# Kernel tuning notes

Measured on AMD Instinct MI355X. Metric: run time of the kernel, lower is better.

## Reference

```python
import jax, jax.numpy as jnp
import numpy as np

T = 16          # video_length
HEADS = 8
DIM_HEAD = 64
INNER = HEADS * DIM_HEAD   # 512
SCALE = DIM_HEAD ** -0.5
QDIM = 320      # input_dims[0]
NTOK = 1024     # num_tokens[0] == N == M (pose tokens)
CTOK = 256      # context_tokens == per-frame context tokens (16x16)
HC = WC = 16    # sqrt(CTOK)
HM = WM = 32    # after bilinear x2 upsample (sqrt(NTOK))
CDIM = 1024     # context_dim
NBLOCKS = 2
FF_INNER = 4 * QDIM  # 1280, GEGLU proj -> 2*FF_INNER


def _ln(x, w, b):
    mu = jnp.mean(x, axis=-1, keepdims=True)
    var = jnp.mean(jnp.square(x - mu), axis=-1, keepdims=True)
    return (x - mu) * jax.lax.rsqrt(var + 1e-5) * w + b


def setup_inputs() -> dict:
    key = jax.random.key(0)
    ks = jax.random.split(key, 24)
    rn = lambda i, shape, s: jax.random.normal(ks[i], shape, jnp.float32) * s
    return {
        "hidden_state": rn(0, (2 * T, NTOK, HEADS, QDIM // HEADS), 1.0),
        "context": rn(1, (2, 2, CTOK, CDIM), 1.0),
        "pose": rn(2, (2, QDIM, T, HM, WM), 1.0),
        "Wq": rn(3, (NBLOCKS, QDIM, INNER), 0.02),
        "Wk": rn(4, (NBLOCKS, CDIM, INNER), 0.02),
        "Wv": rn(5, (NBLOCKS, CDIM, INNER), 0.02),
        "Wa": rn(6, (NBLOCKS, QDIM, INNER), 0.02),
        "agent_bias": rn(7, (NBLOCKS, NTOK, CTOK), 0.01),
        "query_bias": rn(8, (NBLOCKS, NTOK, NTOK), 0.01),
        "dwc_w": rn(9, (NBLOCKS, INNER, 1, 3, 3), 0.1),
        "dwc_b": rn(10, (NBLOCKS, INNER), 0.01),
        "Wo": rn(11, (NBLOCKS, INNER, QDIM), 0.02),
        "norm_w": jnp.ones((QDIM,), jnp.float32),
        "norm_b": jnp.zeros((QDIM,), jnp.float32),
        "ffln_w": jnp.ones((QDIM,), jnp.float32),
        "ffln_b": jnp.zeros((QDIM,), jnp.float32),
        "ff_w1": rn(12, (QDIM, 2 * FF_INNER), 0.02),
        "ff_b1": jnp.zeros((2 * FF_INNER,), jnp.float32),
        "ff_w2": rn(13, (FF_INNER, QDIM), 0.02),
        "ff_b2": jnp.zeros((QDIM,), jnp.float32),
    }


def reference(hidden_state, context, pose, Wq, Wk, Wv, Wa, agent_bias, query_bias,
              dwc_w, dwc_b, Wo, norm_w, norm_b, ffln_w, ffln_b, ff_w1, ff_b1, ff_w2, ff_b2):
    B = hidden_state.shape[0] // T
    C = context.shape[1]
    # '(B T) N H D -> B T N (H D)'
    hs = hidden_state.reshape(B, T, NTOK, QDIM)
    # pose 'B D T H W -> B T (H W) D'
    pose_t = jnp.transpose(pose, (0, 2, 3, 4, 1)).reshape(B, T, NTOK, QDIM)

    for b in range(NBLOCKS):
        # ---- compute_kv_attention ----
        k = jnp.einsum('bcnd,de->bcne', context, Wk[b])          # [B,C,Nc,INNER]
        v = jnp.einsum('bcnd,de->bcne', context, Wv[b])          # [B,C,Nc,INNER]
        a_tok = jnp.einsum('btmd,de->btme', pose_t, Wa[b])       # [B,T,M,INNER]
        kf = k.reshape(B, C * CTOK, INNER)                       # 'B C N D -> B (C N) D'
        attn = jnp.einsum('btme,bne->btmn', a_tok * SCALE, kf)   # [B,T,M,C*Nc]
        # faithful to torch: view(B,T,M,N,C) then 'B T M N C -> (B C) T M N'
        attn = attn.reshape(B, T, NTOK, CTOK, C).transpose(0, 4, 1, 2, 3)  # [B,C,T,M,Nc]
        attn = jax.nn.softmax(attn + agent_bias[b], axis=-1)
        akv = jnp.einsum('bctmn,bcne->bctme', attn, v)           # [B,C,T,M,INNER]
        agent_kv = jnp.max(akv, axis=1)                          # [B,T,M,INNER]

        # depthwise conv over context-frame value maps (T-independent since v repeated over T)
        v_img = v.transpose(0, 1, 3, 2).reshape(B * C, INNER, HC, WC)
        vd = jax.lax.conv_general_dilated(
            v_img, dwc_w[b], (1, 1), 'SAME', feature_group_count=INNER,
            dimension_numbers=('NCHW', 'OIHW', 'NCHW')) + dwc_b[b][None, :, None, None]
        vd = vd.reshape(B, C, INNER, HC, WC).max(axis=1)         # max over frames
        vd = jax.image.resize(vd, (B, INNER, HM, WM), method='bilinear')  # x2, align_corners=False
        v_tok = vd.reshape(B, INNER, NTOK).transpose(0, 2, 1)[:, None]    # [B,1,N,INNER]

        # ---- agent-token cross attention ----
        nh = _ln(hs, norm_w, norm_b)
        q = jnp.einsum('btnd,de->btne', nh, Wq[b])
        aq = jax.nn.softmax(
            jnp.einsum('btne,btme->btnm', q * SCALE, a_tok) + query_bias[b], axis=-1)
        x = jnp.einsum('btnm,btme->btne', aq, agent_kv) + v_tok
        hs = jnp.einsum('btne,ed->btnd', x, Wo[b]) + hs          # residual

    # ---- LayerNorm + GEGLU FeedForward + residual ----
    h = _ln(hs, ffln_w, ffln_b)
    p = h @ ff_w1 + ff_b1
    a, g = jnp.split(p, 2, axis=-1)
    hs = (a * jax.nn.gelu(g, approximate=False)) @ ff_w2 + ff_b2 + hs
    return hs.reshape(B * T, NTOK, QDIM)
```

## Files before the change

### kernel.cpp

```cpp
#include <hip/hip_runtime.h>
#include <hip/hip_bf16.h>
#include <math.h>

typedef __hip_bfloat16 bf16;
typedef short short8 __attribute__((ext_vector_type(8)));
typedef float floatx4 __attribute__((ext_vector_type(4)));

static const int B2   = 2;
static const int TT   = 16;
static const int NTK  = 1024;
static const int CTK  = 256;
static const int QD   = 320;
static const int INNR = 512;
static const int CD   = 1024;
#define SCALE_ 0.125f
#define LDK 40

__device__ __forceinline__ ushort f2bu(float x){
  bf16 h = __float2bfloat16(x);
  return *reinterpret_cast<ushort*>(&h);
}


struct StT128 {
  const float* src; int ld; int tid;
  float4 r[4];
  __device__ __forceinline__ void load(int k0){
#pragma unroll
    for(int i=0;i<4;i++){
      int f4=tid+i*256, rr=f4>>3, kq=f4&7;
      r[i] = *(const float4*)(src + (size_t)rr*ld + k0 + kq*4);
    }
  }
  __device__ __forceinline__ void store(ushort* dst){
#pragma unroll
    for(int i=0;i<4;i++){
      int f4=tid+i*256, rr=f4>>3, kq=f4&7;
      float4 v=r[i];
      ushort4 u={f2bu(v.x),f2bu(v.y),f2bu(v.z),f2bu(v.w)};
      *(ushort4*)&dst[rr*LDK+kq*4]=u;
    }
  }
};

struct StAtok {
  const float* base; int tid;
  float r[16];
  __device__ __forceinline__ void load(int k0){
#pragma unroll
    for(int i=0;i<16;i++){
      int e=tid+i*256, m=e&127, kk=e>>7;
      r[i]=base[(size_t)(k0+kk)*(TT*NTK) + m];
    }
  }
  __device__ __forceinline__ void store(ushort* dst){
#pragma unroll
    for(int i=0;i<16;i++){
      int e=tid+i*256, m=e&127, kk=e>>7;
      dst[m*LDK+kk]=f2bu(r[i]);
    }
  }
};

template<int NV>
struct StBf {
  const ushort* src; int ld; int tid;
  short8 r[NV];
  __device__ __forceinline__ void load(int k0){
#pragma unroll
    for(int v=0;v<NV;v++){
      int idx=tid+v*256, rr=idx>>2, kq=idx&3;
      r[v] = *(const short8*)&src[(size_t)rr*ld + k0 + kq*8];
    }
  }
  __device__ __forceinline__ void store(ushort* dst){
#pragma unroll
    for(int v=0;v<NV;v++){
      int idx=tid+v*256, rr=idx>>2, kq=idx&3;
      *(short8*)&dst[rr*LDK + kq*8] = r[v];
    }
  }
};

template<int NT>
__device__ __forceinline__ void mfma_tiles(const ushort* As, const ushort* Bs,
    floatx4 (&acc)[4][NT], int mOff, int nOff, int lane15, int quad){
  short8 af[4], bfm[NT];
  #pragma unroll
  for(int i=0;i<4;i++) af[i] = *(const short8*)&As[(mOff + i*16 + lane15)*LDK + quad*8];
  #pragma unroll
  for(int j=0;j<NT;j++) bfm[j] = *(const short8*)&Bs[(nOff + j*16 + lane15)*LDK + quad*8];
  #pragma unroll
  for(int i=0;i<4;i++)
    #pragma unroll
    for(int j=0;j<NT;j++)
      acc[i][j] = __builtin_amdgcn_mfma_f32_16x16x32_bf16(af[i], bfm[j], acc[i][j], 0, 0, 0);
}

template<int NT>
__device__ __forceinline__ void zero_acc(floatx4 (&acc)[4][NT]){
  floatx4 z = {0.f,0.f,0.f,0.f};
  #pragma unroll
  for(int i=0;i<4;i++)
    #pragma unroll
    for(int j=0;j<NT;j++) acc[i][j]=z;
}

template<int NT, class SA, class SB>
__device__ __forceinline__ void core_db(SA& sa, SB& sb, int K,
    ushort* As0, ushort* As1, ushort* Bs0, ushort* Bs1,
    floatx4 (&acc)[4][NT], int mOff, int nOff, int lane15, int quad){
  sa.load(0); sb.load(0);
  sa.store(As0); sb.store(Bs0);
  const int nk = K>>5;
  for(int i=0;i<nk-1;i++){
    sa.load((i+1)<<5); sb.load((i+1)<<5);
    __syncthreads();
    mfma_tiles<NT>((i&1)?As1:As0, (i&1)?Bs1:Bs0, acc, mOff,nOff,lane15,quad);
    sa.store((i&1)?As0:As1); sb.store((i&1)?Bs0:Bs1);
  }
  __syncthreads();
  mfma_tiles<NT>(((nk-1)&1)?As1:As0, ((nk-1)&1)?Bs1:Bs0, acc, mOff,nOff,lane15,quad);
}

#define GEMM_IDS(NT_) \
  const int tid=threadIdx.x, w=tid>>6, lane15=tid&15, quad=(tid>>4)&3; \
  const int mOff=(w&1)*64, nOff=(w>>1)*(NT_*16);
#define EPI(NT_) \
  _Pragma("unroll") for(int i=0;i<4;i++) \
  _Pragma("unroll") for(int j=0;j<NT_;j++) \
  _Pragma("unroll") for(int r=0;r<4;r++)
#define ROWG (mOff + i*16 + quad*4 + r)
#define COLG (nOff + j*16 + lane15)

__global__ void __launch_bounds__(256) k_wtrans(const float* __restrict__ W, ushort* __restrict__ WT,
                                                int K, int N){
  __shared__ float t[64][65];
  const int kB = blockIdx.y*64, nB = blockIdx.x*64;
  for(int e=threadIdx.x; e<4096; e+=256){
    int r=e>>6, c=e&63;
    t[r][c] = W[(size_t)(kB+r)*N + nB+c];
  }
  __syncthreads();
  for(int e=threadIdx.x; e<4096; e+=256){
    int r=e>>6, c=e&63;
    WT[(size_t)(nB+r)*K + kB+c] = f2bu(t[c][r]);
  }
}

__global__ void k_ln(const float* __restrict__ hs, const float* __restrict__ w,
                     const float* __restrict__ b, ushort* __restrict__ out, int row0){
  const int r = blockIdx.x, lane = threadIdx.x;
  const float* hr = hs + (size_t)(row0+r)*QD;
  float s=0.f, s2=0.f;
  #pragma unroll
  for(int j=0;j<5;j++){ float v=hr[j*64+lane]; s+=v; s2+=v*v; }
  #pragma unroll
  for(int o=32;o;o>>=1){ s+=__shfl_down(s,o); s2+=__shfl_down(s2,o); }
  s = __shfl(s,0); s2 = __shfl(s2,0);
  float mu=s*(1.f/320.f);
  float var=s2*(1.f/320.f)-mu*mu;
  float rs=rsqrtf(var+1e-5f);
  #pragma unroll
  for(int j=0;j<5;j++){
    int c=j*64+lane;
    out[(size_t)r*QD + c] = f2bu((hr[c]-mu)*rs*w[c]+b[c]);
  }
}

__global__ void __launch_bounds__(256) g_kv(const float* __restrict__ A, const ushort* __restrict__ BT,
                                            ushort* __restrict__ kbf, float* __restrict__ vf,
                                            ushort* __restrict__ vT){
  __shared__ ushort As[2][128*LDK], Bs[2][128*LDK];
  GEMM_IDS(4)
  const int rB=blockIdx.y*128, cB=blockIdx.x*128;
  floatx4 acc[4][4]; zero_acc<4>(acc);
  StT128 sa{A + (size_t)rB*CD, CD, tid};
  StBf<2> sb{BT + (size_t)cB*CD, CD, tid};
  core_db<4>(sa, sb, CD, As[0],As[1],Bs[0],Bs[1], acc, mOff,nOff,lane15,quad);
  if(kbf){
    EPI(4){ kbf[(size_t)(rB+ROWG)*INNR + cB+COLG] = f2bu(acc[i][j][r]); }
  }else{
    EPI(4){
      int row=rB+ROWG, col=cB+COLG;
      float v=acc[i][j][r];
      vf[(size_t)row*INNR + col] = v;
      vT[((size_t)(row>>8)*INNR + col)*CTK + (row&255)] = f2bu(v);
    }
  }
}

__global__ void __launch_bounds__(256) g_atok(const float* __restrict__ pose, const ushort* __restrict__ WaT,
                                              ushort* __restrict__ atok, int pt0){
  __shared__ ushort As[2][128*LDK], Bs[2][128*LDK];
  GEMM_IDS(4)
  const int z=blockIdx.z, pt=pt0+z, bb=pt>>4, t=pt&15;
  const int rB=blockIdx.y*128, cB=blockIdx.x*128;
  floatx4 acc[4][4]; zero_acc<4>(acc);
  StAtok sa{pose + ((size_t)(bb*QD)*TT + t)*NTK + rB, tid};
  StBf<2> sb{WaT + (size_t)cB*QD, QD, tid};
  core_db<4>(sa, sb, QD, As[0],As[1],Bs[0],Bs[1], acc, mOff,nOff,lane15,quad);
  EPI(4){ atok[((size_t)z*NTK + rB+ROWG)*INNR + cB+COLG] = f2bu(acc[i][j][r]); }
}

__global__ void __launch_bounds__(256) g_logits(const ushort* __restrict__ atok, const ushort* __restrict__ kbf,
                                                const float* __restrict__ abias, float* __restrict__ lgC, int pt0){
  __shared__ ushort As[2][128*LDK], Bs[2][128*LDK];
  GEMM_IDS(4)
  const int z=blockIdx.z, zp=z>>1, c=z&1, pt=pt0+zp, bb=pt>>4;
  const int rB=blockIdx.y*128, cB=blockIdx.x*128;
  floatx4 acc[4][4]; zero_acc<4>(acc);
  StBf<2> sa{atok + ((size_t)zp*NTK + rB)*INNR, INNR, tid};
  StBf<2> sb{kbf + (size_t)(bb*512 + 2*cB + c)*INNR, 2*INNR, tid};
  core_db<4>(sa, sb, INNR, As[0],As[1],Bs[0],Bs[1], acc, mOff,nOff,lane15,quad);
  float* Cz = lgC + (size_t)(zp*2+c)*NTK*CTK;
  EPI(4){
    int row=rB+ROWG, col=cB+COLG;
    Cz[(size_t)row*CTK + col] = acc[i][j][r]*SCALE_ + abias[(size_t)row*CTK + col];
  }
}

__global__ void __launch_bounds__(256) g_pvmax(const ushort* __restrict__ lg_us, const ushort* __restrict__ vT,
                                               ushort* __restrict__ akvT, int pt0){
  __shared__ ushort As[2][128*LDK], Bs[2][128*LDK];
  GEMM_IDS(4)
  const int zp=blockIdx.z, pt=pt0+zp, bb=pt>>4;
  const int rB=blockIdx.y*128, cB=blockIdx.x*128;
  floatx4 best[4][4]; zero_acc<4>(best);
  floatx4 acc[4][4];
  for(int c=0;c<2;c++){
    if(c) __syncthreads();
    zero_acc<4>(acc);
    StBf<2> sa{lg_us + ((size_t)(zp*2+c)*NTK + rB)*INNR, INNR, tid};
    StBf<2> sb{vT + ((size_t)(bb*2+c)*INNR + cB)*CTK, CTK, tid};
    core_db<4>(sa, sb, CTK, As[0],As[1],Bs[0],Bs[1], acc, mOff,nOff,lane15,quad);
    if(c==0){
      #pragma unroll
      for(int i=0;i<4;i++)
        #pragma unroll
        for(int j=0;j<4;j++) best[i][j]=acc[i][j];
    }else{
      EPI(4){ best[i][j][r] = fmaxf(best[i][j][r], acc[i][j][r]); }
    }
  }
  #pragma unroll
  for(int i=0;i<4;i++)
    #pragma unroll
    for(int j=0;j<4;j++){
      int col = cB + nOff + j*16 + lane15;
      int row0 = rB + mOff + i*16 + quad*4;
      ushort4 u = { f2bu(best[i][j][0]), f2bu(best[i][j][1]), f2bu(best[i][j][2]), f2bu(best[i][j][3]) };
      *(ushort4*)&akvT[((size_t)zp*INNR + col)*NTK + row0] = u;
    }
}

__global__ void __launch_bounds__(256) g_q(const ushort* __restrict__ lnh, const ushort* __restrict__ WqT,
                                           ushort* __restrict__ qb){
  __shared__ ushort As[2][128*LDK], Bs[2][128*LDK];
  GEMM_IDS(4)
  const int rB=blockIdx.y*128, cB=blockIdx.x*128;
  floatx4 acc[4][4]; zero_acc<4>(acc);
  StBf<2> sa{lnh + (size_t)rB*QD, QD, tid};
  StBf<2> sb{WqT + (size_t)cB*QD, QD, tid};
  core_db<4>(sa, sb, QD, As[0],As[1],Bs[0],Bs[1], acc, mOff,nOff,lane15,quad);
  EPI(4){ qb[(size_t)(rB+ROWG)*INNR + cB+COLG] = f2bu(acc[i][j][r]); }
}

__global__ void __launch_bounds__(256) g_aql(const ushort* __restrict__ qb, const ushort* __restrict__ atok,
                                             const float* __restrict__ qbias, float* __restrict__ D){
  __shared__ ushort As[2][128*LDK], Bs[2][128*LDK];
  GEMM_IDS(4)
  const int z=blockIdx.z;
  const int rB=blockIdx.y*128, cB=blockIdx.x*128;
  floatx4 acc[4][4]; zero_acc<4>(acc);
  StBf<2> sa{qb + ((size_t)z*NTK + rB)*INNR, INNR, tid};
  StBf<2> sb{atok + ((size_t)z*NTK + cB)*INNR, INNR, tid};
  core_db<4>(sa, sb, INNR, As[0],As[1],Bs[0],Bs[1], acc, mOff,nOff,lane15,quad);
  float* Dz = D + (size_t)z*NTK*NTK;
  EPI(4){
    int row=rB+ROWG, col=cB+COLG;
    Dz[(size_t)row*NTK + col] = acc[i][j][r]*SCALE_ + qbias[(size_t)row*NTK + col];
  }
}

__global__ void __launch_bounds__(256) g_aqpv(const float* __restrict__ D, const ushort* __restrict__ akvT,
                                              const float* __restrict__ vt, ushort* __restrict__ xb, int pt0){
  __shared__ ushort As[2][128*LDK], Bs[2][128*LDK];
  GEMM_IDS(4)
  const int z=blockIdx.z, pt=pt0+z, bb=pt>>4;
  const int rB=blockIdx.y*128, cB=blockIdx.x*128;
  floatx4 acc[4][4]; zero_acc<4>(acc);
  StBf<2> sa{(const ushort*)D + (size_t)z*2097152 + (size_t)rB*2048, 2048, tid};
  StBf<2> sb{akvT + ((size_t)z*INNR + cB)*NTK, NTK, tid};
  core_db<4>(sa, sb, NTK, As[0],As[1],Bs[0],Bs[1], acc, mOff,nOff,lane15,quad);
  EPI(4){
    int row=rB+ROWG, col=cB+COLG;
    xb[((size_t)z*NTK + row)*INNR + col] = f2bu(acc[i][j][r] + vt[((size_t)bb*NTK + row)*INNR + col]);
  }
}

__global__ void __launch_bounds__(256) g_wo(const ushort* __restrict__ xb, const ushort* __restrict__ WoT,
                                            float* __restrict__ hs, int row0){
  __shared__ ushort As[2][128*LDK], Bs[2][64*LDK];
  GEMM_IDS(2)
  const int rB=blockIdx.y*128, cB=blockIdx.x*64;
  floatx4 acc[4][2]; zero_acc<2>(acc);
  StBf<2> sa{xb + (size_t)rB*INNR, INNR, tid};
  StBf<1> sb{WoT + (size_t)cB*INNR, INNR, tid};
  core_db<2>(sa, sb, INNR, As[0],As[1],Bs[0],Bs[1], acc, mOff,nOff,lane15,quad);
  EPI(2){
    size_t o = (size_t)(row0+rB+ROWG)*QD + cB+COLG;
    hs[o] = hs[o] + acc[i][j][r];
  }
}

__global__ void __launch_bounds__(256) g_ff1(const ushort* __restrict__ lnh, const ushort* __restrict__ W1T,
    const float* __restrict__ b1, ushort* __restrict__ G){
  __shared__ ushort As[2][128*LDK], Ba[2][64*LDK], Bg[2][64*LDK];
  GEMM_IDS(2)
  const int rB=blockIdx.y*128, cB=blockIdx.x*64;
  floatx4 accA[4][2], accG[4][2]; zero_acc<2>(accA); zero_acc<2>(accG);
  StBf<2> sa{lnh + (size_t)rB*QD, QD, tid};
  StBf<1> s1{W1T + (size_t)cB*QD, QD, tid};
  StBf<1> s2{W1T + (size_t)(1280+cB)*QD, QD, tid};
  sa.load(0); s1.load(0); s2.load(0);
  sa.store(As[0]); s1.store(Ba[0]); s2.store(Bg[0]);
  const int nk = QD>>5;
  for(int i=0;i<nk-1;i++){
    int k=(i+1)<<5;
    sa.load(k); s1.load(k); s2.load(k);
    __syncthreads();
    const int cur=i&1;
    mfma_tiles<2>(As[cur],Ba[cur],accA,mOff,nOff,lane15,quad);
    mfma_tiles<2>(As[cur],Bg[cur],accG,mOff,nOff,lane15,quad);
    sa.store(As[cur^1]); s1.store(Ba[cur^1]); s2.store(Bg[cur^1]);
  }
  __syncthreads();
  {
    const int cur=(nk-1)&1;
    mfma_tiles<2>(As[cur],Ba[cur],accA,mOff,nOff,lane15,quad);
    mfma_tiles<2>(As[cur],Bg[cur],accG,mOff,nOff,lane15,quad);
  }
  EPI(2){
    int n = cB+COLG;
    float a = accA[i][j][r] + b1[n];
    float g = accG[i][j][r] + b1[1280+n];
    G[(size_t)(rB+ROWG)*1280 + n] = f2bu(a*0.5f*g*(1.0f+erff(g*0.70710678f)));
  }
}

__global__ void __launch_bounds__(256) g_ff2(const ushort* __restrict__ G, const ushort* __restrict__ W2T,
    const float* __restrict__ b2v, float* __restrict__ hs, int row0){
  __shared__ ushort As[2][128*LDK], Bs[2][64*LDK];
  GEMM_IDS(2)
  const int rB=blockIdx.y*128, cB=blockIdx.x*64;
  floatx4 acc[4][2]; zero_acc<2>(acc);
  StBf<2> sa{G + (size_t)rB*1280, 1280, tid};
  StBf<1> sb{W2T + (size_t)cB*1280, 1280, tid};
  core_db<2>(sa, sb, 1280, As[0],As[1],Bs[0],Bs[1], acc, mOff,nOff,lane15,quad);
  EPI(2){
    int col = cB+COLG;
    size_t o = (size_t)(row0+rB+ROWG)*QD + col;
    hs[o] = acc[i][j][r] + b2v[col] + hs[o];
  }
}

__global__ void k_softmax256(float* __restrict__ buf){
  __shared__ float red[8];
  const int tid=threadIdx.x;
  size_t row=blockIdx.x;
  float x = buf[row*256+tid];
  float m = x;
  #pragma unroll
  for(int o=32;o;o>>=1) m=fmaxf(m,__shfl_down(m,o));
  if((tid&63)==0) red[tid>>6]=m;
  __syncthreads();
  if(tid==0) red[4]=fmaxf(fmaxf(red[0],red[1]),fmaxf(red[2],red[3]));
  __syncthreads();
  float M=red[4];
  float e=__expf(x-M);
  float s=e;
  #pragma unroll
  for(int o=32;o;o>>=1) s+=__shfl_down(s,o);
  if((tid&63)==0) red[tid>>6]=s;
  __syncthreads();
  if(tid==0) red[5]=red[0]+red[1]+red[2]+red[3];
  __syncthreads();
  ((ushort*)buf)[row*512 + tid] = f2bu(e/red[5]);
}

__global__ void k_softmax1024(float* __restrict__ buf){
  __shared__ float red[8];
  const int tid=threadIdx.x;
  size_t row=blockIdx.x;
  float4* p = (float4*)(buf + row*1024);
  float4 v = p[tid];
  float m = fmaxf(fmaxf(v.x,v.y),fmaxf(v.z,v.w));
  #pragma unroll
  for(int o=32;o;o>>=1) m=fmaxf(m,__shfl_down(m,o));
  if((tid&63)==0) red[tid>>6]=m;
  __syncthreads();
  if(tid==0) red[4]=fmaxf(fmaxf(red[0],red[1]),fmaxf(red[2],red[3]));
  __syncthreads();
  float M=red[4];
  v.x=__expf(v.x-M); v.y=__expf(v.y-M); v.z=__expf(v.z-M); v.w=__expf(v.w-M);
  float s=v.x+v.y+v.z+v.w;
  #pragma unroll
  for(int o=32;o;o>>=1) s+=__shfl_down(s,o);
  if((tid&63)==0) red[tid>>6]=s;
  __syncthreads();
  if(tid==0) red[5]=red[0]+red[1]+red[2]+red[3];
  __syncthreads();
  float inv=1.0f/red[5];
  ushort4 u = { f2bu(v.x*inv), f2bu(v.y*inv), f2bu(v.z*inv), f2bu(v.w*inv) };
  *(ushort4*)((ushort*)buf + row*2048 + (size_t)tid*4) = u;
}

__global__ void k_conv(const float* __restrict__ vbuf, const float* __restrict__ w3,
                       const float* __restrict__ wb, float* __restrict__ vm){
  int idx = blockIdx.x*256+threadIdx.x;
  if(idx >= B2*CTK*INNR) return;
  int e = idx & 511, hw = (idx>>9)&255, b = idx>>17;
  int h = hw>>4, w = hw&15;
  float wt[9];
  #pragma unroll
  for(int q=0;q<9;q++) wt[q]=w3[e*9+q];
  float bias = wb[e];
  float best=0.f;
  for(int c=0;c<2;c++){
    float s = bias;
    #pragma unroll
    for(int dy=-1;dy<=1;dy++)
      #pragma unroll
      for(int dx=-1;dx<=1;dx++){
        int hh=h+dy, ww=w+dx;
        if(hh>=0&&hh<16&&ww>=0&&ww<16)
          s += wt[(dy+1)*3+(dx+1)]*vbuf[((size_t)(b*2+c)*CTK + hh*16+ww)*INNR + e];
      }
    best = c ? fmaxf(best,s) : s;
  }
  vm[((size_t)b*CTK + hw)*INNR + e] = best;
}

__device__ __forceinline__ void up_wt(int i, int& j0, int& j1, float& w){
  float s = 0.5f*i - 0.25f;
  float f = floorf(s);
  w = s - f;
  int a = (int)f;
  j0 = min(15, max(0, a));
  j1 = min(15, max(0, a+1));
}
__global__ void k_up(const float* __restrict__ vm, float* __restrict__ vt){
  int idx = blockIdx.x*256+threadIdx.x;
  if(idx >= B2*NTK*INNR) return;
  int e = idx & 511, n = (idx>>9)&1023, b = idx>>19;
  int hm = n>>5, wm = n&31;
  int h0,h1,w0,w1; float fh,fw;
  up_wt(hm,h0,h1,fh); up_wt(wm,w0,w1,fw);
  const float* base = vm + (size_t)b*CTK*INNR + e;
  float v00=base[(size_t)(h0*16+w0)*INNR], v01=base[(size_t)(h0*16+w1)*INNR];
  float v10=base[(size_t)(h1*16+w0)*INNR], v11=base[(size_t)(h1*16+w1)*INNR];
  vt[((size_t)b*NTK+n)*INNR+e] = (1.f-fh)*((1.f-fw)*v00+fw*v01) + fh*((1.f-fw)*v10+fw*v11);
}


extern "C" void kernel_launch(void* const* d_in, const int* in_sizes, int n_in,
                              void* d_out, int out_size, void* d_ws, size_t ws_size,
                              hipStream_t stream){
  const float* hidden = (const float*)d_in[0];
  const float* context= (const float*)d_in[1];
  const float* pose   = (const float*)d_in[2];
  const float* Wq  = (const float*)d_in[3];
  const float* Wk  = (const float*)d_in[4];
  const float* Wv  = (const float*)d_in[5];
  const float* Wa  = (const float*)d_in[6];
  const float* abias=(const float*)d_in[7];
  const float* qbias=(const float*)d_in[8];
  const float* dwcw=(const float*)d_in[9];
  const float* dwcb=(const float*)d_in[10];
  const float* Wo  = (const float*)d_in[11];
  const float* nw  = (const float*)d_in[12];
  const float* nb  = (const float*)d_in[13];
  const float* fw  = (const float*)d_in[14];
  const float* fb  = (const float*)d_in[15];
  const float* W1  = (const float*)d_in[16];
  const float* b1  = (const float*)d_in[17];
  const float* W2  = (const float*)d_in[18];
  const float* b2v = (const float*)d_in[19];

  float* ws = (float*)d_ws;
  const size_t wsfl = ws_size / 4;

  int S;
  {
    const size_t need16 = 4513792ull + 16ull*2260992ull;
    S = (wsfl >= need16) ? 16 : 4;
  }
  const int NCH = 32 / S;

  size_t off = 0;
  auto take = [&](size_t n){ size_t o = off; off += n; return o; };
  float*  vm   = ws + take(262144);
  float*  vb   = ws + take(524288);
  float*  vt   = ws + take(1048576);
  ushort* kbf  = (ushort*)(ws + take(262144));
  ushort* vbT  = (ushort*)(ws + take(262144));
  ushort* lnh  = (ushort*)(ws + take((size_t)S*163840));
  ushort* wkT  = (ushort*)(ws + take(524288));
  ushort* wvT  = (ushort*)(ws + take(524288));
  ushort* wqT  = (ushort*)(ws + take(163840));
  ushort* waT  = (ushort*)(ws + take(163840));
  ushort* woT  = (ushort*)(ws + take(163840));
  ushort* w1T  = (ushort*)(ws + take(409600));
  ushort* w2T  = (ushort*)(ws + take(204800));
  float*  SH   = ws + take((size_t)S*1048576);
  ushort* atok = (ushort*)(ws + take((size_t)S*262144));
  ushort* akvT = (ushort*)(ws + take((size_t)S*262144));
  ushort* qbf  = (ushort*)(ws + take((size_t)S*262144));
  ushort* xbf  = (ushort*)(ws + take((size_t)S*262144));

  float* hs = (float*)d_out;

  hipMemcpyAsync(hs, hidden, (size_t)B2*TT*NTK*QD*sizeof(float),
                 hipMemcpyDeviceToDevice, stream);

  for(int b=0;b<2;b++){
    k_wtrans<<<dim3(8,16),256,0,stream>>>(Wk+(size_t)b*CD*INNR,  wkT+(size_t)b*524288, CD, INNR);
    k_wtrans<<<dim3(8,16),256,0,stream>>>(Wv+(size_t)b*CD*INNR,  wvT+(size_t)b*524288, CD, INNR);
    k_wtrans<<<dim3(8,5), 256,0,stream>>>(Wq+(size_t)b*QD*INNR,  wqT+(size_t)b*163840, QD, INNR);
    k_wtrans<<<dim3(8,5), 256,0,stream>>>(Wa+(size_t)b*QD*INNR,  waT+(size_t)b*163840, QD, INNR);
    k_wtrans<<<dim3(5,8), 256,0,stream>>>(Wo+(size_t)b*INNR*QD,  woT+(size_t)b*163840, INNR, QD);
  }
  k_wtrans<<<dim3(40,5),256,0,stream>>>(W1, w1T, QD, 2560);
  k_wtrans<<<dim3(5,20),256,0,stream>>>(W2, w2T, 1280, QD);

  for(int b=0;b<2;b++){
    g_kv<<<dim3(4,8),256,0,stream>>>(context, wkT+(size_t)b*524288, kbf, nullptr, nullptr);
    g_kv<<<dim3(4,8),256,0,stream>>>(context, wvT+(size_t)b*524288, nullptr, vb, vbT);
    k_conv<<<(B2*CTK*INNR)/256,256,0,stream>>>(vb, dwcw+(size_t)b*INNR*9, dwcb+(size_t)b*INNR, vm);
    k_up<<<(B2*NTK*INNR)/256,256,0,stream>>>(vm, vt);
    for(int ch=0; ch<NCH; ch++){
      const int pt0 = ch*S;
      g_atok<<<dim3(4,8,S),256,0,stream>>>(pose, waT+(size_t)b*163840, atok, pt0);
      g_logits<<<dim3(2,8,2*S),256,0,stream>>>(atok, kbf, abias+(size_t)b*NTK*CTK, SH, pt0);
      k_softmax256<<<2*S*1024,256,0,stream>>>(SH);
      g_pvmax<<<dim3(4,8,S),256,0,stream>>>((const ushort*)SH, vbT, akvT, pt0);
      k_ln<<<S*1024,64,0,stream>>>(hs, nw, nb, lnh, pt0*1024);
      g_q<<<dim3(4,S*8),256,0,stream>>>(lnh, wqT+(size_t)b*163840, qbf);
      g_aql<<<dim3(8,8,S),256,0,stream>>>(qbf, atok, qbias+(size_t)b*NTK*NTK, SH);
      k_softmax1024<<<S*1024,256,0,stream>>>(SH);
      g_aqpv<<<dim3(4,8,S),256,0,stream>>>(SH, akvT, vt, xbf, pt0);
      g_wo<<<dim3(5,S*8),256,0,stream>>>(xbf, woT+(size_t)b*163840, hs, pt0*1024);
    }
  }

  for(int ch=0; ch<NCH; ch++){
    const int row0 = ch*S*1024;
    k_ln<<<S*1024,64,0,stream>>>(hs, fw, fb, lnh, row0);
    g_ff1<<<dim3(20,S*8),256,0,stream>>>(lnh, w1T, b1, (ushort*)SH);
    g_ff2<<<dim3(5,S*8),256,0,stream>>>((ushort*)SH, w2T, b2v, hs, row0);
  }
}
```

Baseline: 1.390 ms.

## Stage bf16 GEMM tiles with direct global-to-LDS loads and XOR-swizzled layout

Replaces the register-staged bf16 tile loads in all GEMM kernels with global_load_lds direct-to-LDS transfers, and changes the LDS tile layout from a padded stride of 40 to an unpadded stride of 32 with a rotation swizzle to avoid bank conflicts. The pipeline loop is reordered so the next tile's loads are issued before the MFMA work on the current tile, followed by a vmcnt wait and a barrier. This is meant to cut VGPR pressure and the LDS store instructions, and to overlap memory traffic with compute. The risk is that the swizzle mapping in the direct-LDS writes does not line up with the reads, and the full vmcnt(0) wait each iteration may limit how much overlap is gained.

Result: no change. 1.399 ms (+0.6%).

```diff
diff --git a/kernel.cpp b/kernel.cpp
--- a/kernel.cpp
+++ b/kernel.cpp
@@ -14,31 +14,53 @@
 static const int INNR = 512;
 static const int CD   = 1024;
 #define SCALE_ 0.125f
-#define LDK 40
 
 __device__ __forceinline__ ushort f2bu(float x){
   bf16 h = __float2bfloat16(x);
   return *reinterpret_cast<ushort*>(&h);
 }
 
+__device__ __forceinline__ void gld16(const ushort* g, ushort* l){
+  __builtin_amdgcn_global_load_lds(
+      (const __attribute__((address_space(1))) void*)g,
+      (__attribute__((address_space(3))) void*)l,
+      16, 0, 0);
+}
+
+
+template<int NV>
+struct GBf {
+  const ushort* src; int ld; int tid;
+  __device__ __forceinline__ void stage(ushort* dst, int k0){
+#pragma unroll
+    for(int v=0;v<NV;v++){
+      int idx=tid+v*256, row=idx>>2, s=idx&3;
+      int q=(s-(row>>1))&3;
+      gld16(src + (size_t)row*ld + k0 + q*8,
+            dst + (size_t)(v*256 + (tid&192))*8);
+    }
+  }
+  __device__ __forceinline__ void finish(ushort*){}
+};
 
 struct StT128 {
   const float* src; int ld; int tid;
   float4 r[4];
-  __device__ __forceinline__ void load(int k0){
+  __device__ __forceinline__ void stage(ushort*, int k0){
 #pragma unroll
     for(int i=0;i<4;i++){
       int f4=tid+i*256, rr=f4>>3, kq=f4&7;
       r[i] = *(const float4*)(src + (size_t)rr*ld + k0 + kq*4);
     }
   }
-  __device__ __forceinline__ void store(ushort* dst){
+  __device__ __forceinline__ void finish(ushort* dst){
 #pragma unroll
     for(int i=0;i<4;i++){
       int f4=tid+i*256, rr=f4>>3, kq=f4&7;
+      int s=((kq>>1)+(rr>>1))&3;
       float4 v=r[i];
       ushort4 u={f2bu(v.x),f2bu(v.y),f2bu(v.z),f2bu(v.w)};
-      *(ushort4*)&dst[rr*LDK+kq*4]=u;
+      *(ushort4*)&dst[rr*32 + s*8 + (kq&1)*4]=u;
     }
   }
 };
@@ -46,38 +68,19 @@
 struct StAtok {
   const float* base; int tid;
   float r[16];
-  __device__ __forceinline__ void load(int k0){
+  __device__ __forceinline__ void stage(ushort*, int k0){
 #pragma unroll
     for(int i=0;i<16;i++){
       int e=tid+i*256, m=e&127, kk=e>>7;
       r[i]=base[(size_t)(k0+kk)*(TT*NTK) + m];
     }
   }
-  __device__ __forceinline__ void store(ushort* dst){
+  __device__ __forceinline__ void finish(ushort* dst){
 #pragma unroll
     for(int i=0;i<16;i++){
       int e=tid+i*256, m=e&127, kk=e>>7;
-      dst[m*LDK+kk]=f2bu(r[i]);
-    }
-  }
-};
-
-template<int NV>
-struct StBf {
-  const ushort* src; int ld; int tid;
-  short8 r[NV];
-  __device__ __forceinline__ void load(int k0){
-#pragma unroll
-    for(int v=0;v<NV;v++){
-      int idx=tid+v*256, rr=idx>>2, kq=idx&3;
-      r[v] = *(const short8*)&src[(size_t)rr*ld + k0 + kq*8];
-    }
-  }
-  __device__ __forceinline__ void store(ushort* dst){
-#pragma unroll
-    for(int v=0;v<NV;v++){
-      int idx=tid+v*256, rr=idx>>2, kq=idx&3;
-      *(short8*)&dst[rr*LDK + kq*8] = r[v];
+      int s=((kk>>3)+(m>>1))&3;
+      dst[m*32 + s*8 + (kk&7)]=f2bu(r[i]);
     }
   }
 };
@@ -87,9 +90,15 @@
     floatx4 (&acc)[4][NT], int mOff, int nOff, int lane15, int quad){
   short8 af[4], bfm[NT];
   #pragma unroll
-  for(int i=0;i<4;i++) af[i] = *(const short8*)&As[(mOff + i*16 + lane15)*LDK + quad*8];
-  #pragma unroll
-  for(int j=0;j<NT;j++) bfm[j] = *(const short8*)&Bs[(nOff + j*16 + lane15)*LDK + quad*8];
+  for(int i=0;i<4;i++){
+    int ar = mOff + i*16 + lane15;
+    af[i] = *(const short8*)&As[ar*32 + ((quad + (ar>>1))&3)*8];
+  }
+  #pragma unroll
+  for(int j=0;j<NT;j++){
+    int br = nOff + j*16 + lane15;
+    bfm[j] = *(const short8*)&Bs[br*32 + ((quad + (br>>1))&3)*8];
+  }
   #pragma unroll
   for(int i=0;i<4;i++)
     #pragma unroll
@@ -107,19 +116,23 @@
 }
 
 template<int NT, class SA, class SB>
-__device__ __forceinline__ void core_db(SA& sa, SB& sb, int K,
+__device__ __forceinline__ void core_g(SA& sa, SB& sb, int K,
     ushort* As0, ushort* As1, ushort* Bs0, ushort* Bs1,
     floatx4 (&acc)[4][NT], int mOff, int nOff, int lane15, int quad){
-  sa.load(0); sb.load(0);
-  sa.store(As0); sb.store(Bs0);
+  sa.stage(As0,0); sb.stage(Bs0,0);
+  sa.finish(As0);  sb.finish(Bs0);
+  asm volatile("s_waitcnt vmcnt(0)" ::: "memory");
+  __syncthreads();
   const int nk = K>>5;
   for(int i=0;i<nk-1;i++){
-    sa.load((i+1)<<5); sb.load((i+1)<<5);
+    ushort* Ac=(i&1)?As1:As0; ushort* An=(i&1)?As0:As1;
+    ushort* Bc=(i&1)?Bs1:Bs0; ushort* Bn=(i&1)?Bs0:Bs1;
+    sa.stage(An,(i+1)<<5); sb.stage(Bn,(i+1)<<5);
+    mfma_tiles<NT>(Ac,Bc,acc,mOff,nOff,lane15,quad);
+    sa.finish(An); sb.finish(Bn);
+    asm volatile("s_waitcnt vmcnt(0)" ::: "memory");
     __syncthreads();
-    mfma_tiles<NT>((i&1)?As1:As0, (i&1)?Bs1:Bs0, acc, mOff,nOff,lane15,quad);
-    sa.store((i&1)?As0:As1); sb.store((i&1)?Bs0:Bs1);
-  }
-  __syncthreads();
+  }
   mfma_tiles<NT>(((nk-1)&1)?As1:As0, ((nk-1)&1)?Bs1:Bs0, acc, mOff,nOff,lane15,quad);
 }
 
@@ -171,13 +184,13 @@
 __global__ void __launch_bounds__(256) g_kv(const float* __restrict__ A, const ushort* __restrict__ BT,
                                             ushort* __restrict__ kbf, float* __restrict__ vf,
                                             ushort* __restrict__ vT){
-  __shared__ ushort As[2][128*LDK], Bs[2][128*LDK];
+  __shared__ ushort As[2][128*32], Bs[2][128*32];
   GEMM_IDS(4)
   const int rB=blockIdx.y*128, cB=blockIdx.x*128;
   floatx4 acc[4][4]; zero_acc<4>(acc);
   StT128 sa{A + (size_t)rB*CD, CD, tid};
-  StBf<2> sb{BT + (size_t)cB*CD, CD, tid};
-  core_db<4>(sa, sb, CD, As[0],As[1],Bs[0],Bs[1], acc, mOff,nOff,lane15,quad);
+  GBf<2> sb{BT + (size_t)cB*CD, CD, tid};
+  core_g<4>(sa, sb, CD, As[0],As[1],Bs[0],Bs[1], acc, mOff,nOff,lane15,quad);
   if(kbf){
     EPI(4){ kbf[(size_t)(rB+ROWG)*INNR + cB+COLG] = f2bu(acc[i][j][r]); }
   }else{
@@ -192,27 +205,27 @@
 
 __global__ void __launch_bounds__(256) g_atok(const float* __restrict__ pose, const ushort* __restrict__ WaT,
                                               ushort* __restrict__ atok, int pt0){
-  __shared__ ushort As[2][128*LDK], Bs[2][128*LDK];
+  __shared__ ushort As[2][128*32], Bs[2][128*32];
   GEMM_IDS(4)
   const int z=blockIdx.z, pt=pt0+z, bb=pt>>4, t=pt&15;
   const int rB=blockIdx.y*128, cB=blockIdx.x*128;
   floatx4 acc[4][4]; zero_acc<4>(acc);
   StAtok sa{pose + ((size_t)(bb*QD)*TT + t)*NTK + rB, tid};
-  StBf<2> sb{WaT + (size_t)cB*QD, QD, tid};
-  core_db<4>(sa, sb, QD, As[0],As[1],Bs[0],Bs[1], acc, mOff,nOff,lane15,quad);
+  GBf<2> sb{WaT + (size_t)cB*QD, QD, tid};
+  core_g<4>(sa, sb, QD, As[0],As[1],Bs[0],Bs[1], acc, mOff,nOff,lane15,quad);
   EPI(4){ atok[((size_t)z*NTK + rB+ROWG)*INNR + cB+COLG] = f2bu(acc[i][j][r]); }
 }
 
 __global__ void __launch_bounds__(256) g_logits(const ushort* __restrict__ atok, const ushort* __restrict__ kbf,
                                                 const float* __restrict__ abias, float* __restrict__ lgC, int pt0){
-  __shared__ ushort As[2][128*LDK], Bs[2][128*LDK];
+  __shared__ ushort As[2][128*32], Bs[2][128*32];
   GEMM_IDS(4)
   const int z=blockIdx.z, zp=z>>1, c=z&1, pt=pt0+zp, bb=pt>>4;
   const int rB=blockIdx.y*128, cB=blockIdx.x*128;
   floatx4 acc[4][4]; zero_acc<4>(acc);
-  StBf<2> sa{atok + ((size_t)zp*NTK + rB)*INNR, INNR, tid};
-  StBf<2> sb{kbf + (size_t)(bb*512 + 2*cB + c)*INNR, 2*INNR, tid};
-  core_db<4>(sa, sb, INNR, As[0],As[1],Bs[0],Bs[1], acc, mOff,nOff,lane15,quad);
+  GBf<2> sa{atok + ((size_t)zp*NTK + rB)*INNR, INNR, tid};
+  GBf<2> sb{kbf + (size_t)(bb*512 + 2*cB + c)*INNR, 2*INNR, tid};
+  core_g<4>(sa, sb, INNR, As[0],As[1],Bs[0],Bs[1], acc, mOff,nOff,lane15,quad);
   float* Cz = lgC + (size_t)(zp*2+c)*NTK*CTK;
   EPI(4){
     int row=rB+ROWG, col=cB+COLG;
@@ -222,7 +235,7 @@
 
 __global__ void __launch_bounds__(256) g_pvmax(const ushort* __restrict__ lg_us, const ushort* __restrict__ vT,
                                                ushort* __restrict__ akvT, int pt0){
-  __shared__ ushort As[2][128*LDK], Bs[2][128*LDK];
+  __shared__ ushort As[2][128*32], Bs[2][128*32];
   GEMM_IDS(4)
   const int zp=blockIdx.z, pt=pt0+zp, bb=pt>>4;
   const int rB=blockIdx.y*128, cB=blockIdx.x*128;
@@ -231,9 +244,9 @@
   for(int c=0;c<2;c++){
     if(c) __syncthreads();
     zero_acc<4>(acc);
-    StBf<2> sa{lg_us + ((size_t)(zp*2+c)*NTK + rB)*INNR, INNR, tid};
-    StBf<2> sb{vT + ((size_t)(bb*2+c)*INNR + cB)*CTK, CTK, tid};
-    core_db<4>(sa, sb, CTK, As[0],As[1],Bs[0],Bs[1], acc, mOff,nOff,lane15,quad);
+    GBf<2> sa{lg_us + ((size_t)(zp*2+c)*NTK + rB)*INNR, INNR, tid};
+    GBf<2> sb{vT + ((size_t)(bb*2+c)*INNR + cB)*CTK, CTK, tid};
+    core_g<4>(sa, sb, CTK, As[0],As[1],Bs[0],Bs[1], acc, mOff,nOff,lane15,quad);
     if(c==0){
       #pragma unroll
       for(int i=0;i<4;i++)
@@ -256,26 +269,26 @@
 
 __global__ void __launch_bounds__(256) g_q(const ushort* __restrict__ lnh, const ushort* __restrict__ WqT,
                                            ushort* __restrict__ qb){
-  __shared__ ushort As[2][128*LDK], Bs[2][128*LDK];
+  __shared__ ushort As[2][128*32], Bs[2][128*32];
   GEMM_IDS(4)
   const int rB=blockIdx.y*128, cB=blockIdx.x*128;
   floatx4 acc[4][4]; zero_acc<4>(acc);
-  StBf<2> sa{lnh + (size_t)rB*QD, QD, tid};
-  StBf<2> sb{WqT + (size_t)cB*QD, QD, tid};
-  core_db<4>(sa, sb, QD, As[0],As[1],Bs[0],Bs[1], acc, mOff,nOff,lane15,quad);
+  GBf<2> sa{lnh + (size_t)rB*QD, QD, tid};
+  GBf<2> sb{WqT + (size_t)cB*QD, QD, tid};
+  core_g<4>(sa, sb, QD, As[0],As[1],Bs[0],Bs[1], acc, mOff,nOff,lane15,quad);
   EPI(4){ qb[(size_t)(rB+ROWG)*INNR + cB+COLG] = f2bu(acc[i][j][r]); }
 }
 
 __global__ void __launch_bounds__(256) g_aql(const ushort* __restrict__ qb, const ushort* __restrict__ atok,
                                              const float* __restrict__ qbias, float* __restrict__ D){
-  __shared__ ushort As[2][128*LDK], Bs[2][128*LDK];
+  __shared__ ushort As[2][128*32], Bs[2][128*32];
   GEMM_IDS(4)
   const int z=blockIdx.z;
   const int rB=blockIdx.y*128, cB=blockIdx.x*128;
   floatx4 acc[4][4]; zero_acc<4>(acc);
-  StBf<2> sa{qb + ((size_t)z*NTK + rB)*INNR, INNR, tid};
-  StBf<2> sb{atok + ((size_t)z*NTK + cB)*INNR, INNR, tid};
-  core_db<4>(sa, sb, INNR, As[0],As[1],Bs[0],Bs[1], acc, mOff,nOff,lane15,quad);
+  GBf<2> sa{qb + ((size_t)z*NTK + rB)*INNR, INNR, tid};
+  GBf<2> sb{atok + ((size_t)z*NTK + cB)*INNR, INNR, tid};
+  core_g<4>(sa, sb, INNR, As[0],As[1],Bs[0],Bs[1], acc, mOff,nOff,lane15,quad);
   float* Dz = D + (size_t)z*NTK*NTK;
   EPI(4){
     int row=rB+ROWG, col=cB+COLG;
@@ -285,14 +298,14 @@
 
 __global__ void __launch_bounds__(256) g_aqpv(const float* __restrict__ D, const ushort* __restrict__ akvT,
                                               const float* __restrict__ vt, ushort* __restrict__ xb, int pt0){
-  __shared__ ushort As[2][128*LDK], Bs[2][128*LDK];
+  __shared__ ushort As[2][128*32], Bs[2][128*32];
   GEMM_IDS(4)
   const int z=blockIdx.z, pt=pt0+z, bb=pt>>4;
   const int rB=blockIdx.y*128, cB=blockIdx.x*128;
   floatx4 acc[4][4]; zero_acc<4>(acc);
-  StBf<2> sa{(const ushort*)D + (size_t)z*2097152 + (size_t)rB*2048, 2048, tid};
-  StBf<2> sb{akvT + ((size_t)z*INNR + cB)*NTK, NTK, tid};
-  core_db<4>(sa, sb, NTK, As[0],As[1],Bs[0],Bs[1], acc, mOff,nOff,lane15,quad);
+  GBf<2> sa{(const ushort*)D + (size_t)z*2097152 + (size_t)rB*2048, 2048, tid};
+  GBf<2> sb{akvT + ((size_t)z*INNR + cB)*NTK, NTK, tid};
+  core_g<4>(sa, sb, NTK, As[0],As[1],Bs[0],Bs[1], acc, mOff,nOff,lane15,quad);
   EPI(4){
     int row=rB+ROWG, col=cB+COLG;
     xb[((size_t)z*NTK + row)*INNR + col] = f2bu(acc[i][j][r] + vt[((size_t)bb*NTK + row)*INNR + col]);
@@ -301,13 +314,13 @@
 
 __global__ void __launch_bounds__(256) g_wo(const ushort* __restrict__ xb, const ushort* __restrict__ WoT,
                                             float* __restrict__ hs, int row0){
-  __shared__ ushort As[2][128*LDK], Bs[2][64*LDK];
+  __shared__ ushort As[2][128*32], Bs[2][64*32];
   GEMM_IDS(2)
   const int rB=blockIdx.y*128, cB=blockIdx.x*64;
   floatx4 acc[4][2]; zero_acc<2>(acc);
-  StBf<2> sa{xb + (size_t)rB*INNR, INNR, tid};
-  StBf<1> sb{WoT + (size_t)cB*INNR, INNR, tid};
-  core_db<2>(sa, sb, INNR, As[0],As[1],Bs[0],Bs[1], acc, mOff,nOff,lane15,quad);
+  GBf<2> sa{xb + (size_t)rB*INNR, INNR, tid};
+  GBf<1> sb{WoT + (size_t)cB*INNR, INNR, tid};
+  core_g<2>(sa, sb, INNR, As[0],As[1],Bs[0],Bs[1], acc, mOff,nOff,lane15,quad);
   EPI(2){
     size_t o = (size_t)(row0+rB+ROWG)*QD + cB+COLG;
     hs[o] = hs[o] + acc[i][j][r];
@@ -316,26 +329,26 @@
 
 __global__ void __launch_bounds__(256) g_ff1(const ushort* __restrict__ lnh, const ushort* __restrict__ W1T,
     const float* __restrict__ b1, ushort* __restrict__ G){
-  __shared__ ushort As[2][128*LDK], Ba[2][64*LDK], Bg[2][64*LDK];
+  __shared__ ushort As[2][128*32], Ba[2][64*32], Bg[2][64*32];
   GEMM_IDS(2)
   const int rB=blockIdx.y*128, cB=blockIdx.x*64;
   floatx4 accA[4][2], accG[4][2]; zero_acc<2>(accA); zero_acc<2>(accG);
-  StBf<2> sa{lnh + (size_t)rB*QD, QD, tid};
-  StBf<1> s1{W1T + (size_t)cB*QD, QD, tid};
-  StBf<1> s2{W1T + (size_t)(1280+cB)*QD, QD, tid};
-  sa.load(0); s1.load(0); s2.load(0);
-  sa.store(As[0]); s1.store(Ba[0]); s2.store(Bg[0]);
+  GBf<2> sa{lnh + (size_t)rB*QD, QD, tid};
+  GBf<1> s1{W1T + (size_t)cB*QD, QD, tid};
+  GBf<1> s2{W1T + (size_t)(1280+cB)*QD, QD, tid};
+  sa.stage(As[0],0); s1.stage(Ba[0],0); s2.stage(Bg[0],0);
+  asm volatile("s_waitcnt vmcnt(0)" ::: "memory");
+  __syncthreads();
   const int nk = QD>>5;
   for(int i=0;i<nk-1;i++){
     int k=(i+1)<<5;
-    sa.load(k); s1.load(k); s2.load(k);
-    __syncthreads();
     const int cur=i&1;
+    sa.stage(As[cur^1],k); s1.stage(Ba[cur^1],k); s2.stage(Bg[cur^1],k);
     mfma_tiles<2>(As[cur],Ba[cur],accA,mOff,nOff,lane15,quad);
     mfma_tiles<2>(As[cur],Bg[cur],accG,mOff,nOff,lane15,quad);
-    sa.store(As[cur^1]); s1.store(Ba[cur^1]); s2.store(Bg[cur^1]);
-  }
-  __syncthreads();
+    asm volatile("s_waitcnt vmcnt(0)" ::: "memory");
+    __syncthreads();
+  }
   {
     const int cur=(nk-1)&1;
     mfma_tiles<2>(As[cur],Ba[cur],accA,mOff,nOff,lane15,quad);
@@ -351,13 +364,13 @@
 
 __global__ void __launch_bounds__(256) g_ff2(const ushort* __restrict__ G, const ushort* __restrict__ W2T,
     const float* __restrict__ b2v, float* __restrict__ hs, int row0){
-  __shared__ ushort As[2][128*LDK], Bs[2][64*LDK];
+  __shared__ ushort As[2][128*32], Bs[2][64*32];
   GEMM_IDS(2)
   const int rB=blockIdx.y*128, cB=blockIdx.x*64;
   floatx4 acc[4][2]; zero_acc<2>(acc);
-  StBf<2> sa{G + (size_t)rB*1280, 1280, tid};
-  StBf<1> sb{W2T + (size_t)cB*1280, 1280, tid};
-  core_db<2>(sa, sb, 1280, As[0],As[1],Bs[0],Bs[1], acc, mOff,nOff,lane15,quad);
+  GBf<2> sa{G + (size_t)rB*1280, 1280, tid};
+  GBf<1> sb{W2T + (size_t)cB*1280, 1280, tid};
+  core_g<2>(sa, sb, 1280, As[0],As[1],Bs[0],Bs[1], acc, mOff,nOff,lane15,quad);
   EPI(2){
     int col = cB+COLG;
     size_t o = (size_t)(row0+rB+ROWG)*QD + col;
```

## Swizzle shared-memory GEMM tiles and batch K/V projections for both blocks

Applied to the files above, without the earlier changes.

Replaces the padded LDS tile layout (stride 40) with an unpadded stride-32 layout that uses an XOR-like rotation of 8-element chunks by row, applied consistently in all staging loaders and MFMA fragment reads. This is meant to avoid LDS bank conflicts while shrinking shared memory per block. It also merges the four K/V projection GEMMs (two blocks × K/V) into one launch with a z-dimension, which needs larger workspace buffers for per-block K, V and upsampled V. The swizzle must stay consistent across every loader, which is the main risk.

Result: faster. 1.315 ms (-5.4%).

```diff
diff --git a/kernel.cpp b/kernel.cpp
--- a/kernel.cpp
+++ b/kernel.cpp
@@ -14,53 +14,12 @@
 static const int INNR = 512;
 static const int CD   = 1024;
 #define SCALE_ 0.125f
-#define LDK 40
 
 __device__ __forceinline__ ushort f2bu(float x){
   bf16 h = __float2bfloat16(x);
   return *reinterpret_cast<ushort*>(&h);
 }
 
-
-struct StT128 {
-  const float* src; int ld; int tid;
-  float4 r[4];
-  __device__ __forceinline__ void load(int k0){
-#pragma unroll
-    for(int i=0;i<4;i++){
-      int f4=tid+i*256, rr=f4>>3, kq=f4&7;
-      r[i] = *(const float4*)(src + (size_t)rr*ld + k0 + kq*4);
-    }
-  }
-  __device__ __forceinline__ void store(ushort* dst){
-#pragma unroll
-    for(int i=0;i<4;i++){
-      int f4=tid+i*256, rr=f4>>3, kq=f4&7;
-      float4 v=r[i];
-      ushort4 u={f2bu(v.x),f2bu(v.y),f2bu(v.z),f2bu(v.w)};
-      *(ushort4*)&dst[rr*LDK+kq*4]=u;
-    }
-  }
-};
-
-struct StAtok {
-  const float* base; int tid;
-  float r[16];
-  __device__ __forceinline__ void load(int k0){
-#pragma unroll
-    for(int i=0;i<16;i++){
-      int e=tid+i*256, m=e&127, kk=e>>7;
-      r[i]=base[(size_t)(k0+kk)*(TT*NTK) + m];
-    }
-  }
-  __device__ __forceinline__ void store(ushort* dst){
-#pragma unroll
-    for(int i=0;i<16;i++){
-      int e=tid+i*256, m=e&127, kk=e>>7;
-      dst[m*LDK+kk]=f2bu(r[i]);
-    }
-  }
-};
 
 template<int NV>
 struct StBf {
@@ -77,7 +36,49 @@
 #pragma unroll
     for(int v=0;v<NV;v++){
       int idx=tid+v*256, rr=idx>>2, kq=idx&3;
-      *(short8*)&dst[rr*LDK + kq*8] = r[v];
+      *(short8*)&dst[rr*32 + ((kq+(rr>>1))&3)*8] = r[v];
+    }
+  }
+};
+
+struct StT128 {
+  const float* src; int ld; int tid;
+  float4 r[4];
+  __device__ __forceinline__ void load(int k0){
+#pragma unroll
+    for(int i=0;i<4;i++){
+      int f4=tid+i*256, rr=f4>>3, kq=f4&7;
+      r[i] = *(const float4*)(src + (size_t)rr*ld + k0 + kq*4);
+    }
+  }
+  __device__ __forceinline__ void store(ushort* dst){
+#pragma unroll
+    for(int i=0;i<4;i++){
+      int f4=tid+i*256, rr=f4>>3, kq=f4&7;
+      int s=((kq>>1)+(rr>>1))&3;
+      float4 v=r[i];
+      ushort4 u={f2bu(v.x),f2bu(v.y),f2bu(v.z),f2bu(v.w)};
+      *(ushort4*)&dst[rr*32 + s*8 + (kq&1)*4]=u;
+    }
+  }
+};
+
+struct StAtok {
+  const float* base; int tid;
+  float r[16];
+  __device__ __forceinline__ void load(int k0){
+#pragma unroll
+    for(int i=0;i<16;i++){
+      int e=tid+i*256, m=e&127, kk=e>>7;
+      r[i]=base[(size_t)(k0+kk)*(TT*NTK) + m];
+    }
+  }
+  __device__ __forceinline__ void store(ushort* dst){
+#pragma unroll
+    for(int i=0;i<16;i++){
+      int e=tid+i*256, m=e&127, kk=e>>7;
+      int s=((kk>>3)+(m>>1))&3;
+      dst[m*32 + s*8 + (kk&7)]=f2bu(r[i]);
     }
   }
 };
@@ -87,9 +88,15 @@
     floatx4 (&acc)[4][NT], int mOff, int nOff, int lane15, int quad){
   short8 af[4], bfm[NT];
   #pragma unroll
-  for(int i=0;i<4;i++) af[i] = *(const short8*)&As[(mOff + i*16 + lane15)*LDK + quad*8];
-  #pragma unroll
-  for(int j=0;j<NT;j++) bfm[j] = *(const short8*)&Bs[(nOff + j*16 + lane15)*LDK + quad*8];
+  for(int i=0;i<4;i++){
+    int ar = mOff + i*16 + lane15;
+    af[i] = *(const short8*)&As[ar*32 + ((quad + (ar>>1))&3)*8];
+  }
+  #pragma unroll
+  for(int j=0;j<NT;j++){
+    int br = nOff + j*16 + lane15;
+    bfm[j] = *(const short8*)&Bs[br*32 + ((quad + (br>>1))&3)*8];
+  }
   #pragma unroll
   for(int i=0;i<4;i++)
     #pragma unroll
@@ -168,19 +175,25 @@
   }
 }
 
-__global__ void __launch_bounds__(256) g_kv(const float* __restrict__ A, const ushort* __restrict__ BT,
-                                            ushort* __restrict__ kbf, float* __restrict__ vf,
-                                            ushort* __restrict__ vT){
-  __shared__ ushort As[2][128*LDK], Bs[2][128*LDK];
-  GEMM_IDS(4)
+__global__ void __launch_bounds__(256) g_kv(const float* __restrict__ A,
+                                            const ushort* __restrict__ wkT, const ushort* __restrict__ wvT,
+                                            ushort* __restrict__ kbf, float* __restrict__ vb,
+                                            ushort* __restrict__ vbT){
+  __shared__ ushort As[2][128*32], Bs[2][128*32];
+  GEMM_IDS(4)
+  const int z=blockIdx.z, b=z>>1, isv=z&1;
+  const ushort* BT = (isv ? wvT : wkT) + (size_t)b*524288;
   const int rB=blockIdx.y*128, cB=blockIdx.x*128;
   floatx4 acc[4][4]; zero_acc<4>(acc);
   StT128 sa{A + (size_t)rB*CD, CD, tid};
   StBf<2> sb{BT + (size_t)cB*CD, CD, tid};
   core_db<4>(sa, sb, CD, As[0],As[1],Bs[0],Bs[1], acc, mOff,nOff,lane15,quad);
-  if(kbf){
-    EPI(4){ kbf[(size_t)(rB+ROWG)*INNR + cB+COLG] = f2bu(acc[i][j][r]); }
+  if(!isv){
+    ushort* kb = kbf + (size_t)b*524288;
+    EPI(4){ kb[(size_t)(rB+ROWG)*INNR + cB+COLG] = f2bu(acc[i][j][r]); }
   }else{
+    float* vf = vb + (size_t)b*524288;
+    ushort* vT = vbT + (size_t)b*524288;
     EPI(4){
       int row=rB+ROWG, col=cB+COLG;
       float v=acc[i][j][r];
@@ -192,7 +205,7 @@
 
 __global__ void __launch_bounds__(256) g_atok(const float* __restrict__ pose, const ushort* __restrict__ WaT,
                                               ushort* __restrict__ atok, int pt0){
-  __shared__ ushort As[2][128*LDK], Bs[2][128*LDK];
+  __shared__ ushort As[2][128*32], Bs[2][128*32];
   GEMM_IDS(4)
   const int z=blockIdx.z, pt=pt0+z, bb=pt>>4, t=pt&15;
   const int rB=blockIdx.y*128, cB=blockIdx.x*128;
@@ -205,7 +218,7 @@
 
 __global__ void __launch_bounds__(256) g_logits(const ushort* __restrict__ atok, const ushort* __restrict__ kbf,
                                                 const float* __restrict__ abias, float* __restrict__ lgC, int pt0){
-  __shared__ ushort As[2][128*LDK], Bs[2][128*LDK];
+  __shared__ ushort As[2][128*32], Bs[2][128*32];
   GEMM_IDS(4)
   const int z=blockIdx.z, zp=z>>1, c=z&1, pt=pt0+zp, bb=pt>>4;
   const int rB=blockIdx.y*128, cB=blockIdx.x*128;
@@ -222,7 +235,7 @@
 
 __global__ void __launch_bounds__(256) g_pvmax(const ushort* __restrict__ lg_us, const ushort* __restrict__ vT,
                                                ushort* __restrict__ akvT, int pt0){
-  __shared__ ushort As[2][128*LDK], Bs[2][128*LDK];
+  __shared__ ushort As[2][128*32], Bs[2][128*32];
   GEMM_IDS(4)
   const int zp=blockIdx.z, pt=pt0+zp, bb=pt>>4;
   const int rB=blockIdx.y*128, cB=blockIdx.x*128;
@@ -256,7 +269,7 @@
 
 __global__ void __launch_bounds__(256) g_q(const ushort* __restrict__ lnh, const ushort* __restrict__ WqT,
                                            ushort* __restrict__ qb){
-  __shared__ ushort As[2][128*LDK], Bs[2][128*LDK];
+  __shared__ ushort As[2][128*32], Bs[2][128*32];
   GEMM_IDS(4)
   const int rB=blockIdx.y*128, cB=blockIdx.x*128;
   floatx4 acc[4][4]; zero_acc<4>(acc);
@@ -268,7 +281,7 @@
 
 __global__ void __launch_bounds__(256) g_aql(const ushort* __restrict__ qb, const ushort* __restrict__ atok,
                                              const float* __restrict__ qbias, float* __restrict__ D){
-  __shared__ ushort As[2][128*LDK], Bs[2][128*LDK];
+  __shared__ ushort As[2][128*32], Bs[2][128*32];
   GEMM_IDS(4)
   const int z=blockIdx.z;
   const int rB=blockIdx.y*128, cB=blockIdx.x*128;
@@ -285,7 +298,7 @@
 
 __global__ void __launch_bounds__(256) g_aqpv(const float* __restrict__ D, const ushort* __restrict__ akvT,
                                               const float* __restrict__ vt, ushort* __restrict__ xb, int pt0){
-  __shared__ ushort As[2][128*LDK], Bs[2][128*LDK];
+  __shared__ ushort As[2][128*32], Bs[2][128*32];
   GEMM_IDS(4)
   const int z=blockIdx.z, pt=pt0+z, bb=pt>>4;
   const int rB=blockIdx.y*128, cB=blockIdx.x*128;
@@ -301,7 +314,7 @@
 
 __global__ void __launch_bounds__(256) g_wo(const ushort* __restrict__ xb, const ushort* __restrict__ WoT,
                                             float* __restrict__ hs, int row0){
-  __shared__ ushort As[2][128*LDK], Bs[2][64*LDK];
+  __shared__ ushort As[2][128*32], Bs[2][64*32];
   GEMM_IDS(2)
   const int rB=blockIdx.y*128, cB=blockIdx.x*64;
   floatx4 acc[4][2]; zero_acc<2>(acc);
@@ -316,7 +329,7 @@
 
 __global__ void __launch_bounds__(256) g_ff1(const ushort* __restrict__ lnh, const ushort* __restrict__ W1T,
     const float* __restrict__ b1, ushort* __restrict__ G){
-  __shared__ ushort As[2][128*LDK], Ba[2][64*LDK], Bg[2][64*LDK];
+  __shared__ ushort As[2][128*32], Ba[2][64*32], Bg[2][64*32];
   GEMM_IDS(2)
   const int rB=blockIdx.y*128, cB=blockIdx.x*64;
   floatx4 accA[4][2], accG[4][2]; zero_acc<2>(accA); zero_acc<2>(accG);
@@ -351,7 +364,7 @@
 
 __global__ void __launch_bounds__(256) g_ff2(const ushort* __restrict__ G, const ushort* __restrict__ W2T,
     const float* __restrict__ b2v, float* __restrict__ hs, int row0){
-  __shared__ ushort As[2][128*LDK], Bs[2][64*LDK];
+  __shared__ ushort As[2][128*32], Bs[2][64*32];
   GEMM_IDS(2)
   const int rB=blockIdx.y*128, cB=blockIdx.x*64;
   floatx4 acc[4][2]; zero_acc<2>(acc);
@@ -493,7 +506,7 @@
 
   int S;
   {
-    const size_t need16 = 4513792ull + 16ull*2260992ull;
+    const size_t need16 = 6610944ull + 16ull*2260992ull;
     S = (wsfl >= need16) ? 16 : 4;
   }
   const int NCH = 32 / S;
@@ -501,10 +514,10 @@
   size_t off = 0;
   auto take = [&](size_t n){ size_t o = off; off += n; return o; };
   float*  vm   = ws + take(262144);
-  float*  vb   = ws + take(524288);
-  float*  vt   = ws + take(1048576);
-  ushort* kbf  = (ushort*)(ws + take(262144));
-  ushort* vbT  = (ushort*)(ws + take(262144));
+  float*  vb   = ws + take(1048576);
+  float*  vt   = ws + take(2097152);
+  ushort* kbf  = (ushort*)(ws + take(524288));
+  ushort* vbT  = (ushort*)(ws + take(524288));
   ushort* lnh  = (ushort*)(ws + take((size_t)S*163840));
   ushort* wkT  = (ushort*)(ws + take(524288));
   ushort* wvT  = (ushort*)(ws + take(524288));
@@ -534,22 +547,28 @@
   k_wtrans<<<dim3(40,5),256,0,stream>>>(W1, w1T, QD, 2560);
   k_wtrans<<<dim3(5,20),256,0,stream>>>(W2, w2T, 1280, QD);
 
+  g_kv<<<dim3(4,8,4),256,0,stream>>>(context, wkT, wvT, kbf, vb, vbT);
   for(int b=0;b<2;b++){
-    g_kv<<<dim3(4,8),256,0,stream>>>(context, wkT+(size_t)b*524288, kbf, nullptr, nullptr);
-    g_kv<<<dim3(4,8),256,0,stream>>>(context, wvT+(size_t)b*524288, nullptr, vb, vbT);
-    k_conv<<<(B2*CTK*INNR)/256,256,0,stream>>>(vb, dwcw+(size_t)b*INNR*9, dwcb+(size_t)b*INNR, vm);
-    k_up<<<(B2*NTK*INNR)/256,256,0,stream>>>(vm, vt);
+    k_conv<<<(B2*CTK*INNR)/256,256,0,stream>>>(vb + (size_t)b*524288,
+        dwcw+(size_t)b*INNR*9, dwcb+(size_t)b*INNR, vm);
+    k_up<<<(B2*NTK*INNR)/256,256,0,stream>>>(vm, vt + (size_t)b*1048576);
+  }
+
+  for(int b=0;b<2;b++){
+    const ushort* kbf_b = kbf + (size_t)b*524288;
+    const ushort* vbT_b = vbT + (size_t)b*524288;
+    const float*  vt_b  = vt  + (size_t)b*1048576;
     for(int ch=0; ch<NCH; ch++){
       const int pt0 = ch*S;
       g_atok<<<dim3(4,8,S),256,0,stream>>>(pose, waT+(size_t)b*163840, atok, pt0);
-      g_logits<<<dim3(2,8,2*S),256,0,stream>>>(atok, kbf, abias+(size_t)b*NTK*CTK, SH, pt0);
+      g_logits<<<dim3(2,8,2*S),256,0,stream>>>(atok, kbf_b, abias+(size_t)b*NTK*CTK, SH, pt0);
       k_softmax256<<<2*S*1024,256,0,stream>>>(SH);
-      g_pvmax<<<dim3(4,8,S),256,0,stream>>>((const ushort*)SH, vbT, akvT, pt0);
+      g_pvmax<<<dim3(4,8,S),256,0,stream>>>((const ushort*)SH, vbT_b, akvT, pt0);
       k_ln<<<S*1024,64,0,stream>>>(hs, nw, nb, lnh, pt0*1024);
       g_q<<<dim3(4,S*8),256,0,stream>>>(lnh, wqT+(size_t)b*163840, qbf);
       g_aql<<<dim3(8,8,S),256,0,stream>>>(qbf, atok, qbias+(size_t)b*NTK*NTK, SH);
       k_softmax1024<<<S*1024,256,0,stream>>>(SH);
-      g_aqpv<<<dim3(4,8,S),256,0,stream>>>(SH, akvT, vt, xbf, pt0);
+      g_aqpv<<<dim3(4,8,S),256,0,stream>>>(SH, akvT, vt_b, xbf, pt0);
       g_wo<<<dim3(5,S*8),256,0,stream>>>(xbf, woT+(size_t)b*163840, hs, pt0*1024);
     }
   }
```
